# Performance work log

Measured on AMD Instinct MI355X. Metric: run time of the kernel, lower is better.

Reference implementation:

```python
import jax, jax.numpy as jnp
import numpy as np

N = 100000
F_IN = 256
F_HID = 256
F_OUT = 40
E = 3200000


def setup_inputs() -> dict:
    key = jax.random.key(0)
    ks = jax.random.split(key, 8)
    x = jax.random.normal(ks[0], (N, F_IN), dtype=jnp.float32)
    edge_index = jax.random.randint(ks[1], (2, E), 0, N, dtype=jnp.int64)
    s1 = 1.0 / np.sqrt(F_IN)
    s2 = 1.0 / np.sqrt(F_HID)
    W1 = jax.random.uniform(ks[2], (F_IN, F_HID), jnp.float32, -s1, s1)
    b1 = jnp.zeros((F_HID,), jnp.float32)
    W2 = jax.random.uniform(ks[3], (F_HID, F_HID), jnp.float32, -s2, s2)
    b2 = jnp.zeros((F_HID,), jnp.float32)
    Wlin = jax.random.uniform(ks[4], (F_HID, F_OUT), jnp.float32, -s2, s2)
    blin = jax.random.uniform(ks[5], (F_OUT,), jnp.float32, -s2, s2)
    return {"x": x, "edge_index": edge_index, "W1": W1, "b1": b1,
            "W2": W2, "b2": b2, "Wlin": Wlin, "blin": blin}


def _gcn_conv(x, src, dst, deg_inv_sqrt, W, b):
    # PyG GCNConv: linear transform, then sym-normalized aggregation, then bias
    h = x @ W                                    # [N, F]
    coef = deg_inv_sqrt[src] * deg_inv_sqrt[dst]  # [E+N]
    msgs = h[src] * coef[:, None]                # gather + scale
    agg = jax.ops.segment_sum(msgs, dst, num_segments=x.shape[0])
    return agg + b


def reference(x, edge_index, W1, b1, W2, b2, Wlin, blin):
    n = x.shape[0]
    # add self-loops (static shape: E + N)
    loops = jnp.arange(n, dtype=edge_index.dtype)
    src = jnp.concatenate([edge_index[0], loops])
    dst = jnp.concatenate([edge_index[1], loops])
    deg = jax.ops.segment_sum(jnp.ones_like(dst, dtype=x.dtype), dst, num_segments=n)
    deg_inv_sqrt = jnp.where(deg > 0, jax.lax.rsqrt(deg), 0.0)
    # dropout is identity in eval mode (training=False)
    h = _gcn_conv(x, src, dst, deg_inv_sqrt, W1, b1)
    h = _gcn_conv(h, src, dst, deg_inv_sqrt, W2, b2)
    logits = h @ Wlin + blin
    return jax.nn.log_softmax(logits, axis=1)
```

## Files before the change

kernel.cpp:

```cpp
#include <hip/hip_runtime.h>
#include <hip/hip_bf16.h>

#define FDIM 256
#define FOUT 40
#define RPB 256

typedef __attribute__((ext_vector_type(8))) short short8;
typedef __attribute__((ext_vector_type(4))) float floatx4;

__device__ __forceinline__ float bf2f(unsigned short u) {
  unsigned int x = ((unsigned int)u) << 16;
  float f;
  __builtin_memcpy(&f, &x, 4);
  return f;
}
__device__ __forceinline__ unsigned short f2bf(float f) {
  __hip_bfloat16 h = __float2bfloat16(f);
  unsigned short u;
  __builtin_memcpy(&u, &h, 2);
  return u;
}


__global__ void detect_k(const int* __restrict__ raw, int nwords, int* __restrict__ flag) {
  if (threadIdx.x == 0) *flag = 0;
  __syncthreads();
  int found = 0;
  for (int w = 1 + 2 * threadIdx.x; w < nwords; w += 512)
    if (raw[w] != 0) { found = 1; break; }
  if (found) atomicOr(flag, 1);
}

__global__ void normalize_k(const int* __restrict__ raw, const int* __restrict__ flag,
                            int* __restrict__ srcN, int* __restrict__ dstN, int e) {
  int i = blockIdx.x * 256 + threadIdx.x;
  if (i >= e) return;
  if (*flag) {
    srcN[i] = raw[i];
    dstN[i] = raw[e + i];
  } else {
    srcN[i] = raw[2 * i];
    dstN[i] = raw[2 * (e + i)];
  }
}


__global__ void zero_cnt_k(int* cnt, int n) {
  int i = blockIdx.x * 256 + threadIdx.x;
  if (i < n) cnt[i] = 0;
}

__global__ void count_k(const int* __restrict__ dst, int* __restrict__ cnt, int e, int n) {
  int i = blockIdx.x * 256 + threadIdx.x;
  if (i < e) {
    int d = dst[i];
    if (d >= 0 && d < n) atomicAdd(&cnt[d], 1);
  }
}

__global__ void dis_leg_k(const int* __restrict__ cnt, float* __restrict__ dis, int n) {
  int i = blockIdx.x * 256 + threadIdx.x;
  if (i < n) dis[i] = rsqrtf((float)cnt[i] + 1.0f);
}

__global__ void scan_a_k(const int* __restrict__ cnt, int* __restrict__ excl,
                         int* __restrict__ bsum, int n) {
  __shared__ int sh[1024];
  int t = threadIdx.x;
  int gid = blockIdx.x * 1024 + t;
  int v = (gid < n) ? cnt[gid] : 0;
  sh[t] = v;
  __syncthreads();
  for (int off = 1; off < 1024; off <<= 1) {
    int x = (t >= off) ? sh[t - off] : 0;
    __syncthreads();
    sh[t] += x;
    __syncthreads();
  }
  if (gid < n) excl[gid] = sh[t] - v;
  if (t == 1023) bsum[blockIdx.x] = sh[1023];
}

__global__ void scan_b_k(int* __restrict__ bsum, int nb) {
  __shared__ int sh[1024];
  int t = threadIdx.x;
  int v = (t < nb) ? bsum[t] : 0;
  sh[t] = v;
  __syncthreads();
  for (int off = 1; off < 1024; off <<= 1) {
    int x = (t >= off) ? sh[t - off] : 0;
    __syncthreads();
    sh[t] += x;
    __syncthreads();
  }
  if (t < nb) bsum[t] = sh[t] - v;
}

__global__ void scan_c_k(int* __restrict__ row_ptr, const int* __restrict__ bsum,
                         const int* __restrict__ cnt, int* __restrict__ cursor, int n) {
  int gid = blockIdx.x * 1024 + threadIdx.x;
  if (gid < n) {
    int r = row_ptr[gid] + bsum[blockIdx.x];
    row_ptr[gid] = r;
    cursor[gid] = r;
    if (gid == n - 1) row_ptr[n] = r + cnt[gid];
  }
}

__global__ void fill_k(const int* __restrict__ src, const int* __restrict__ dst,
                       int* __restrict__ cursor, int* __restrict__ col, int e, int n) {
  int i = blockIdx.x * 256 + threadIdx.x;
  if (i < e) {
    int d = dst[i];
    if (d >= 0 && d < n) {
      int slot = atomicAdd(&cursor[d], 1);
      int s = src[i];
      s = min(max(s, 0), n - 1);
      col[slot] = s;
    }
  }
}


__global__ __launch_bounds__(512) void zerob_k(int* __restrict__ bcnt, int nbuck) {
  int t = threadIdx.x;
  if (t < nbuck) bcnt[t] = 0;
}

__global__ __launch_bounds__(256) void bhist_k(
    const int* __restrict__ raw, const int* __restrict__ flag,
    int* __restrict__ bcnt, int e, int n, int nbuck, int cpb) {
  __shared__ int hist[512];
  int t = threadIdx.x;
  for (int b = t; b < nbuck; b += 256) hist[b] = 0;
  __syncthreads();
  int fl = *flag;
  int start = blockIdx.x * cpb;
  int endc = min(e, start + cpb);
  for (int i = start + t; i < endc; i += 256) {
    int d = fl ? raw[e + i] : raw[2 * (e + i)];
    if (d >= 0 && d < n) atomicAdd(&hist[d >> 8], 1);
  }
  __syncthreads();
  for (int b = t; b < nbuck; b += 256)
    if (hist[b]) atomicAdd(&bcnt[b], hist[b]);
}

__global__ __launch_bounds__(512) void bscan_k(
    const int* __restrict__ bcnt, int* __restrict__ bbase,
    int* __restrict__ bcur, int nbuck) {
  __shared__ int sh[512];
  int t = threadIdx.x;
  int v = (t < nbuck) ? bcnt[t] : 0;
  sh[t] = v;
  __syncthreads();
  for (int off = 1; off < 512; off <<= 1) {
    int x = (t >= off) ? sh[t - off] : 0;
    __syncthreads();
    sh[t] += x;
    __syncthreads();
  }
  if (t < nbuck) {
    int ex = sh[t] - v;
    bbase[t] = ex;
    bcur[t] = ex;
  }
  if (t == nbuck - 1) bbase[nbuck] = sh[t];
}

__global__ __launch_bounds__(1024) void bin2_k(
    const int* __restrict__ raw, const int* __restrict__ flag,
    int* __restrict__ bcur, unsigned int* __restrict__ binned,
    int e, int n, int nbuck, int cpb) {
  __shared__ int hist[512];
  __shared__ int base_[512];
  __shared__ int cnt2[512];
  int t = threadIdx.x;
  int fl = *flag;
  int start = blockIdx.x * cpb;
  int endc = min(e, start + cpb);
  for (int b = t; b < nbuck; b += 1024) { hist[b] = 0; cnt2[b] = 0; }
  __syncthreads();
  for (int i = start + t; i < endc; i += 1024) {
    int d = fl ? raw[e + i] : raw[2 * (e + i)];
    if (d >= 0 && d < n) atomicAdd(&hist[d >> 8], 1);
  }
  __syncthreads();
  for (int b = t; b < nbuck; b += 1024) {
    int h = hist[b];
    base_[b] = h ? atomicAdd(&bcur[b], h) : 0;
  }
  __syncthreads();
  for (int i = start + t; i < endc; i += 1024) {
    int d = fl ? raw[e + i] : raw[2 * (e + i)];
    if (d >= 0 && d < n) {
      int s = fl ? raw[i] : raw[2 * i];
      s = min(max(s, 0), n - 1);
      int bk = d >> 8;
      int pos = base_[bk] + atomicAdd(&cnt2[bk], 1);
      binned[pos] = (((unsigned int)(d & 255)) << 17) | (unsigned int)s;
    }
  }
}

__global__ __launch_bounds__(256) void scatcnt_k(
    const unsigned int* __restrict__ binned, const int* __restrict__ bbase,
    int* __restrict__ row_ptr, float* __restrict__ dis,
    int* __restrict__ col, int n) {
  __shared__ int cnt[RPB];
  __shared__ int sc[RPB];
  __shared__ int cur[RPB];
  int b = blockIdx.x;
  int r0 = b * RPB;
  int r1 = min(n, r0 + RPB);
  int nr = r1 - r0;
  int t = threadIdx.x;
  cnt[t] = 0;
  __syncthreads();
  int e0 = bbase[b], e1 = bbase[b + 1];
  for (int i = e0 + t; i < e1; i += 256)
    atomicAdd(&cnt[binned[i] >> 17], 1);
  __syncthreads();
  int v = cnt[t];
  if (t < nr) dis[r0 + t] = rsqrtf((float)v + 1.0f);
  sc[t] = v;
  __syncthreads();
  for (int off = 1; off < 256; off <<= 1) {
    int x = (t >= off) ? sc[t - off] : 0;
    __syncthreads();
    sc[t] += x;
    __syncthreads();
  }
  int base = e0 + sc[t] - v;
  cur[t] = base;
  if (t < nr) row_ptr[r0 + t] = base;
  if (t == 0 && r1 == n) row_ptr[n] = e1;
  __syncthreads();
  for (int i = e0 + t; i < e1; i += 256) {
    unsigned int p = binned[i];
    int dlow = (int)(p >> 17);
    int slot = atomicAdd(&cur[dlow], 1);
    col[slot] = (int)(p & 0x1FFFF);
  }
}


__global__ __launch_bounds__(64) void wc_k(const float* __restrict__ W2,
                                           const float* __restrict__ Wlin,
                                           float* __restrict__ Wc) {
  __shared__ float row[FDIM];
  int k = blockIdx.x, t = threadIdx.x;
  for (int j = t; j < FDIM; j += 64) row[j] = W2[(size_t)k * FDIM + j];
  __syncthreads();
  if (t < FOUT) {
    float acc = 0.f;
    for (int j = 0; j < FDIM; ++j) acc += row[j] * Wlin[(size_t)j * FOUT + t];
    Wc[(size_t)k * FOUT + t] = acc;
  }
}

__global__ __launch_bounds__(64) void wfull_k(const float* __restrict__ W1,
                                              const float* __restrict__ Wc,
                                              float* __restrict__ Wfull) {
  __shared__ float row[FDIM];
  int k = blockIdx.x, t = threadIdx.x;
  for (int j = t; j < FDIM; j += 64) row[j] = W1[(size_t)k * FDIM + j];
  __syncthreads();
  if (t < FOUT) {
    float acc = 0.f;
    for (int j = 0; j < FDIM; ++j) acc += row[j] * Wc[(size_t)j * FOUT + t];
    Wfull[(size_t)k * FOUT + t] = acc;
  }
}

__global__ __launch_bounds__(64) void rvec_k(const float* __restrict__ b1,
                                             const float* __restrict__ Wc,
                                             const float* __restrict__ b2,
                                             const float* __restrict__ Wlin,
                                             const float* __restrict__ blin,
                                             float* __restrict__ b1c,
                                             float* __restrict__ r2) {
  int t = threadIdx.x;
  if (t < FOUT) {
    float a = 0.f, b = blin[t];
    for (int j = 0; j < FDIM; ++j) {
      a += b1[j] * Wc[(size_t)j * FOUT + t];
      b += b2[j] * Wlin[(size_t)j * FOUT + t];
    }
    b1c[t] = a;
    r2[t] = b;
  }
}

__global__ void wft_k(const float* __restrict__ Wfull, unsigned short* __restrict__ WfT) {
  int o = blockIdx.x, k = threadIdx.x;
  WfT[(size_t)o * FDIM + k] = (o < FOUT) ? f2bf(Wfull[(size_t)k * FOUT + o]) : (unsigned short)0;
}


__global__ __launch_bounds__(256) void proj_k(
    const float* __restrict__ X, const unsigned short* __restrict__ WfT,
    const float* __restrict__ dis, float* __restrict__ Ys, int M) {
  __shared__ __align__(16) unsigned short Asm[64 * 40];
  __shared__ __align__(16) unsigned short Bsm[48 * 264];
  int t = threadIdx.x;
  int block_m = blockIdx.x * 64;
  int lane = t & 63, wave = t >> 6;
  int q = lane >> 4, rcol = lane & 15;
  for (int idx = t; idx < 48 * 256; idx += 256) {
    int o = idx >> 8, k = idx & 255;
    Bsm[o * 264 + k] = WfT[(size_t)o * FDIM + k];
  }
  floatx4 acc[3] = {};
  int arow = t >> 2, cc = (t & 3) * 8;
  int gm = block_m + arow;
  for (int kk = 0; kk < FDIM; kk += 32) {
    __syncthreads();
    {
      float4 v0 = {0, 0, 0, 0}, v1 = {0, 0, 0, 0};
      if (gm < M) {
        v0 = *(const float4*)(X + (size_t)gm * FDIM + kk + cc);
        v1 = *(const float4*)(X + (size_t)gm * FDIM + kk + cc + 4);
      }
      short8 pk;
      pk[0] = (short)f2bf(v0.x); pk[1] = (short)f2bf(v0.y);
      pk[2] = (short)f2bf(v0.z); pk[3] = (short)f2bf(v0.w);
      pk[4] = (short)f2bf(v1.x); pk[5] = (short)f2bf(v1.y);
      pk[6] = (short)f2bf(v1.z); pk[7] = (short)f2bf(v1.w);
      *(short8*)(Asm + arow * 40 + cc) = pk;
    }
    __syncthreads();
    short8 af = *(const short8*)(Asm + (wave * 16 + rcol) * 40 + q * 8);
    short8 b0 = *(const short8*)(Bsm + (rcol)*264 + kk + q * 8);
    short8 b1f = *(const short8*)(Bsm + (16 + rcol) * 264 + kk + q * 8);
    short8 b2f = *(const short8*)(Bsm + (32 + rcol) * 264 + kk + q * 8);
    acc[0] = __builtin_amdgcn_mfma_f32_16x16x32_bf16(af, b0, acc[0], 0, 0, 0);
    acc[1] = __builtin_amdgcn_mfma_f32_16x16x32_bf16(af, b1f, acc[1], 0, 0, 0);
    acc[2] = __builtin_amdgcn_mfma_f32_16x16x32_bf16(af, b2f, acc[2], 0, 0, 0);
  }
#pragma unroll
  for (int rr = 0; rr < 4; ++rr) {
    int m = block_m + wave * 16 + q * 4 + rr;
    if (m >= M) continue;
    float sc = dis[m];
    float* orow = Ys + (size_t)m * FOUT;
    orow[rcol] = acc[0][rr] * sc;
    orow[16 + rcol] = acc[1][rr] * sc;
    if (rcol < 8) orow[32 + rcol] = acc[2][rr] * sc;
  }
}


__global__ __launch_bounds__(256) void agg1_k(
    const float* __restrict__ T, const int* __restrict__ row_ptr,
    const int* __restrict__ col, const float* __restrict__ dis,
    const float* __restrict__ b1c, float* __restrict__ O, int n) {
  int wave = threadIdx.x >> 6, lane = threadIdx.x & 63;
  int wid = blockIdx.x * 4 + wave;
  int nw = gridDim.x * 4;
  bool act = lane < FOUT;
  float bv = act ? b1c[lane] : 0.f;
  for (int i = wid; i < n; i += nw) {
    float a = act ? T[(size_t)i * FOUT + lane] : 0.f;
    int beg = row_ptr[i], end = row_ptr[i + 1];
    for (int j0 = beg; j0 < end; j0 += 64) {
      int jj = j0 + lane;
      int cs = (jj < end) ? col[jj] : 0;
      int cc = min(64, end - j0);
      for (int k = 0; k < cc; k += 16) {
        int sl[16];
        float w[16];
#pragma unroll
        for (int u = 0; u < 16; ++u) {
          int ku = k + u;
          sl[u] = __builtin_amdgcn_readlane(cs, ku & 63);
          w[u] = (ku < cc) ? 1.f : 0.f;
        }
        float g[16];
#pragma unroll
        for (int u = 0; u < 16; ++u)
          g[u] = act ? T[(size_t)sl[u] * FOUT + lane] : 0.f;
#pragma unroll
        for (int u = 0; u < 16; ++u) a = fmaf(w[u], g[u], a);
      }
    }
    if (act) {
      float di = dis[i];
      O[(size_t)i * FOUT + lane] = (di * a + bv) * di;
    }
  }
}


__global__ __launch_bounds__(256) void agg2_k(
    const float* __restrict__ T, const int* __restrict__ row_ptr,
    const int* __restrict__ col, const float* __restrict__ dis,
    const float* __restrict__ r2, float* __restrict__ out, int n) {
  int wave = threadIdx.x >> 6, lane = threadIdx.x & 63;
  int wid = blockIdx.x * 4 + wave;
  int nw = gridDim.x * 4;
  bool act = lane < FOUT;
  float rv = act ? r2[lane] : 0.f;
  for (int i = wid; i < n; i += nw) {
    float a = act ? T[(size_t)i * FOUT + lane] : 0.f;
    int beg = row_ptr[i], end = row_ptr[i + 1];
    for (int j0 = beg; j0 < end; j0 += 64) {
      int jj = j0 + lane;
      int cs = (jj < end) ? col[jj] : 0;
      int cc = min(64, end - j0);
      for (int k = 0; k < cc; k += 16) {
        int sl[16];
        float w[16];
#pragma unroll
        for (int u = 0; u < 16; ++u) {
          int ku = k + u;
          sl[u] = __builtin_amdgcn_readlane(cs, ku & 63);
          w[u] = (ku < cc) ? 1.f : 0.f;
        }
        float g[16];
#pragma unroll
        for (int u = 0; u < 16; ++u)
          g[u] = act ? T[(size_t)sl[u] * FOUT + lane] : 0.f;
#pragma unroll
        for (int u = 0; u < 16; ++u) a = fmaf(w[u], g[u], a);
      }
    }
    float di = dis[i];
    float v = act ? (di * a + rv) : -3.4e38f;
    float m = v;
#pragma unroll
    for (int off = 32; off; off >>= 1) m = fmaxf(m, __shfl_xor(m, off));
    float e = act ? __expf(v - m) : 0.f;
    float s = e;
#pragma unroll
    for (int off = 32; off; off >>= 1) s += __shfl_xor(s, off);
    float lg = m + __logf(s);
    if (act) out[(size_t)i * FOUT + lane] = v - lg;
  }
}


extern "C" void kernel_launch(void* const* d_in, const int* in_sizes, int n_in,
                              void* d_out, int out_size, void* d_ws, size_t ws_size,
                              hipStream_t stream) {
  const float* x   = (const float*)d_in[0];
  const int* eraw  = (const int*)d_in[1];
  const float* W1  = (const float*)d_in[2];
  const float* b1  = (const float*)d_in[3];
  const float* W2  = (const float*)d_in[4];
  const float* b2  = (const float*)d_in[5];
  const float* Wl  = (const float*)d_in[6];
  const float* bl  = (const float*)d_in[7];
  float* out = (float*)d_out;

  const int N = in_sizes[0] / FDIM;
  const int E = in_sizes[1] / 2;

  char* w = (char*)d_ws;
  size_t off = 0;
  auto take = [&](size_t bytes) {
    void* p = w + off;
    off = (off + bytes + 255) & ~(size_t)255;
    return p;
  };
  int* cnt     = (int*)take((size_t)N * 4);
  int* cursor  = (int*)take((size_t)N * 4);
  int* row_ptr = (int*)take((size_t)(N + 1) * 4);
  float* dis   = (float*)take((size_t)N * 4);
  int* bsum    = (int*)take(4096);
  int* eflag   = (int*)take(256);
  int* bcnt    = (int*)take(512 * 4);
  int* bbase   = (int*)take(513 * 4);
  int* bcur    = (int*)take(512 * 4);
  float* Wc    = (float*)take((size_t)FDIM * FOUT * 4);
  float* Wfull = (float*)take((size_t)FDIM * FOUT * 4);
  unsigned short* WfT = (unsigned short*)take((size_t)48 * FDIM * 2);
  float* b1c   = (float*)take(256);
  float* r2    = (float*)take(256);
  int* colx    = (int*)take((size_t)E * 4);

  size_t pairBytes = (size_t)2 * E * 4;
  size_t tabBytes  = (size_t)N * FOUT * 4;
  size_t rABytes = pairBytes > tabBytes ? pairBytes : tabBytes;
  char* regionA = (char*)take(rABytes);
  int* srcN = (int*)regionA;
  int* dstN = srcN + E;
  float* Ys = (float*)regionA;
  size_t binBytes = (size_t)E * 4;
  size_t rBBytes = binBytes > tabBytes ? binBytes : tabBytes;
  char* regionB = (char*)take(rBBytes);
  unsigned int* binned = (unsigned int*)regionB;
  float* Z1s = (float*)regionB;
  (void)n_in; (void)out_size; (void)ws_size;

  int gE = (E + 255) / 256;
  int gN = (N + 255) / 256;
  int NB = (N + 1023) / 1024;
  int gP = (N + 63) / 64;
  int nbuck = (N + RPB - 1) / RPB;
  bool bucketed = (N <= (1 << 17));

  int probe_words = 65536 < 2 * E ? 65536 : 2 * E;
  hipLaunchKernelGGL(detect_k, dim3(1), dim3(256), 0, stream, eraw, probe_words, eflag);

  if (bucketed) {
    int nblk = 256;
    int cpb = (E + nblk - 1) / nblk;
    hipLaunchKernelGGL(zerob_k, dim3(1), dim3(512), 0, stream, bcnt, nbuck);
    hipLaunchKernelGGL(bhist_k, dim3(nblk), dim3(256), 0, stream,
                       eraw, eflag, bcnt, E, N, nbuck, cpb);
    hipLaunchKernelGGL(bscan_k, dim3(1), dim3(512), 0, stream, bcnt, bbase, bcur, nbuck);
    hipLaunchKernelGGL(bin2_k, dim3(nblk), dim3(1024), 0, stream,
                       eraw, eflag, bcur, binned, E, N, nbuck, cpb);
    hipLaunchKernelGGL(scatcnt_k, dim3(nbuck), dim3(256), 0, stream,
                       binned, bbase, row_ptr, dis, colx, N);
  } else {
    hipLaunchKernelGGL(normalize_k, dim3(gE), dim3(256), 0, stream, eraw, eflag, srcN, dstN, E);
    hipLaunchKernelGGL(zero_cnt_k, dim3(gN), dim3(256), 0, stream, cnt, N);
    hipLaunchKernelGGL(count_k, dim3(gE), dim3(256), 0, stream, dstN, cnt, E, N);
    hipLaunchKernelGGL(dis_leg_k, dim3(gN), dim3(256), 0, stream, cnt, dis, N);
    hipLaunchKernelGGL(scan_a_k, dim3(NB), dim3(1024), 0, stream, cnt, row_ptr, bsum, N);
    hipLaunchKernelGGL(scan_b_k, dim3(1), dim3(1024), 0, stream, bsum, NB);
    hipLaunchKernelGGL(scan_c_k, dim3(NB), dim3(1024), 0, stream, row_ptr, bsum, cnt, cursor, N);
    hipLaunchKernelGGL(fill_k, dim3(gE), dim3(256), 0, stream, srcN, dstN, cursor, colx, E, N);
  }

  hipLaunchKernelGGL(wc_k, dim3(FDIM), dim3(64), 0, stream, W2, Wl, Wc);
  hipLaunchKernelGGL(wfull_k, dim3(FDIM), dim3(64), 0, stream, W1, Wc, Wfull);
  hipLaunchKernelGGL(rvec_k, dim3(1), dim3(64), 0, stream, b1, Wc, b2, Wl, bl, b1c, r2);
  hipLaunchKernelGGL(wft_k, dim3(48), dim3(FDIM), 0, stream, Wfull, WfT);

  hipLaunchKernelGGL(proj_k, dim3(gP), dim3(256), 0, stream, x, WfT, dis, Ys, N);
  hipLaunchKernelGGL(agg1_k, dim3(2048), dim3(256), 0, stream,
                     Ys, row_ptr, colx, dis, b1c, Z1s, N);
  hipLaunchKernelGGL(agg2_k, dim3(2048), dim3(256), 0, stream,
                     Z1s, row_ptr, colx, dis, r2, out, N);
}
```

Baseline: 514.9 us.

## Store projected node tables in bf16 and gather three edges per wave step

Measured after the change: 463.8 us. 1.11x faster.

```diff
diff --git a/kernel.cpp b/kernel.cpp
--- a/kernel.cpp
+++ b/kernel.cpp
@@ -19,6 +19,12 @@
   unsigned short u;
   __builtin_memcpy(&u, &h, 2);
   return u;
+}
+__device__ __forceinline__ float blo(unsigned int v) {
+  unsigned int x = v << 16; float f; __builtin_memcpy(&f, &x, 4); return f;
+}
+__device__ __forceinline__ float bhi(unsigned int v) {
+  unsigned int x = v & 0xFFFF0000u; float f; __builtin_memcpy(&f, &x, 4); return f;
 }
 
 
@@ -300,7 +306,7 @@
 
 __global__ __launch_bounds__(256) void proj_k(
     const float* __restrict__ X, const unsigned short* __restrict__ WfT,
-    const float* __restrict__ dis, float* __restrict__ Ys, int M) {
+    const float* __restrict__ dis, unsigned int* __restrict__ Ys32, int M) {
   __shared__ __align__(16) unsigned short Asm[64 * 40];
   __shared__ __align__(16) unsigned short Bsm[48 * 264];
   int t = threadIdx.x;
@@ -338,104 +344,176 @@
     acc[1] = __builtin_amdgcn_mfma_f32_16x16x32_bf16(af, b1f, acc[1], 0, 0, 0);
     acc[2] = __builtin_amdgcn_mfma_f32_16x16x32_bf16(af, b2f, acc[2], 0, 0, 0);
   }
+  __syncthreads();
 #pragma unroll
   for (int rr = 0; rr < 4; ++rr) {
-    int m = block_m + wave * 16 + q * 4 + rr;
-    if (m >= M) continue;
-    float sc = dis[m];
-    float* orow = Ys + (size_t)m * FOUT;
-    orow[rcol] = acc[0][rr] * sc;
-    orow[16 + rcol] = acc[1][rr] * sc;
-    if (rcol < 8) orow[32 + rcol] = acc[2][rr] * sc;
+    int ml = wave * 16 + q * 4 + rr;
+    int m = block_m + ml;
+    float sc = (m < M) ? dis[m] : 0.f;
+    unsigned short* lrow = Asm + ml * 40;
+    lrow[rcol] = f2bf(acc[0][rr] * sc);
+    lrow[16 + rcol] = f2bf(acc[1][rr] * sc);
+    if (rcol < 8) lrow[32 + rcol] = f2bf(acc[2][rr] * sc);
+  }
+  __syncthreads();
+  const unsigned int* A32 = (const unsigned int*)Asm;
+  for (int idx = t; idx < 64 * 20; idx += 256) {
+    int r = idx / 20, c = idx - r * 20;
+    int m = block_m + r;
+    if (m < M) Ys32[(size_t)m * 20 + c] = A32[idx];
   }
 }
 
 
 __global__ __launch_bounds__(256) void agg1_k(
-    const float* __restrict__ T, const int* __restrict__ row_ptr,
+    const unsigned int* __restrict__ T32, const int* __restrict__ row_ptr,
     const int* __restrict__ col, const float* __restrict__ dis,
-    const float* __restrict__ b1c, float* __restrict__ O, int n) {
+    const float* __restrict__ b1c, unsigned int* __restrict__ O32, int n) {
   int wave = threadIdx.x >> 6, lane = threadIdx.x & 63;
   int wid = blockIdx.x * 4 + wave;
   int nw = gridDim.x * 4;
-  bool act = lane < FOUT;
-  float bv = act ? b1c[lane] : 0.f;
+  int e = lane / 20;
+  int fp = lane - e * 20;
+  if (e > 2) { e = 2; fp = 19; }
+  bool e0 = (e == 0), e1 = (e == 1);
+  bool g0 = e0;
+  float2 bv = ((const float2*)b1c)[fp];
   for (int i = wid; i < n; i += nw) {
-    float a = act ? T[(size_t)i * FOUT + lane] : 0.f;
+    unsigned int sv = T32[(size_t)i * 20 + fp];
+    float a0 = g0 ? blo(sv) : 0.f;
+    float a1 = g0 ? bhi(sv) : 0.f;
     int beg = row_ptr[i], end = row_ptr[i + 1];
     for (int j0 = beg; j0 < end; j0 += 64) {
       int jj = j0 + lane;
       int cs = (jj < end) ? col[jj] : 0;
       int cc = min(64, end - j0);
-      for (int k = 0; k < cc; k += 16) {
-        int sl[16];
-        float w[16];
-#pragma unroll
-        for (int u = 0; u < 16; ++u) {
-          int ku = k + u;
-          sl[u] = __builtin_amdgcn_readlane(cs, ku & 63);
-          w[u] = (ku < cc) ? 1.f : 0.f;
+      int kf = cc - cc % 24;
+      int k = 0;
+      for (; k < kf; k += 24) {
+        int sel[8];
+#pragma unroll
+        for (int u = 0; u < 8; ++u) {
+          int sa = __builtin_amdgcn_readlane(cs, k + 3 * u);
+          int sb = __builtin_amdgcn_readlane(cs, k + 3 * u + 1);
+          int sc2 = __builtin_amdgcn_readlane(cs, k + 3 * u + 2);
+          sel[u] = e0 ? sa : (e1 ? sb : sc2);
         }
-        float g[16];
-#pragma unroll
-        for (int u = 0; u < 16; ++u)
-          g[u] = act ? T[(size_t)sl[u] * FOUT + lane] : 0.f;
-#pragma unroll
-        for (int u = 0; u < 16; ++u) a = fmaf(w[u], g[u], a);
+        unsigned int g[8];
+#pragma unroll
+        for (int u = 0; u < 8; ++u) g[u] = T32[(size_t)sel[u] * 20 + fp];
+#pragma unroll
+        for (int u = 0; u < 8; ++u) { a0 += blo(g[u]); a1 += bhi(g[u]); }
       }
-    }
-    if (act) {
+      if (k < cc) {
+        int sel[8];
+        float w[8];
+#pragma unroll
+        for (int u = 0; u < 8; ++u) {
+          int kb = k + 3 * u;
+          int sa = __builtin_amdgcn_readlane(cs, kb & 63);
+          int sb = __builtin_amdgcn_readlane(cs, (kb + 1) & 63);
+          int sc2 = __builtin_amdgcn_readlane(cs, (kb + 2) & 63);
+          sel[u] = e0 ? sa : (e1 ? sb : sc2);
+          w[u] = (kb + e < cc) ? 1.f : 0.f;
+        }
+        unsigned int g[8];
+#pragma unroll
+        for (int u = 0; u < 8; ++u) g[u] = T32[(size_t)sel[u] * 20 + fp];
+#pragma unroll
+        for (int u = 0; u < 8; ++u) {
+          a0 = fmaf(w[u], blo(g[u]), a0);
+          a1 = fmaf(w[u], bhi(g[u]), a1);
+        }
+      }
+    }
+    a0 += __shfl(a0, fp + 20) + __shfl(a0, fp + 40);
+    a1 += __shfl(a1, fp + 20) + __shfl(a1, fp + 40);
+    if (g0) {
       float di = dis[i];
-      O[(size_t)i * FOUT + lane] = (di * a + bv) * di;
-    }
-  }
-}
-
+      unsigned int p = (unsigned int)f2bf((di * a0 + bv.x) * di) |
+                       ((unsigned int)f2bf((di * a1 + bv.y) * di) << 16);
+      O32[(size_t)i * 20 + fp] = p;
+    }
+  }
+}
 
 __global__ __launch_bounds__(256) void agg2_k(
-    const float* __restrict__ T, const int* __restrict__ row_ptr,
+    const unsigned int* __restrict__ T32, const int* __restrict__ row_ptr,
     const int* __restrict__ col, const float* __restrict__ dis,
     const float* __restrict__ r2, float* __restrict__ out, int n) {
   int wave = threadIdx.x >> 6, lane = threadIdx.x & 63;
   int wid = blockIdx.x * 4 + wave;
   int nw = gridDim.x * 4;
-  bool act = lane < FOUT;
-  float rv = act ? r2[lane] : 0.f;
+  int e = lane / 20;
+  int fp = lane - e * 20;
+  if (e > 2) { e = 2; fp = 19; }
+  bool e0 = (e == 0), e1 = (e == 1);
+  bool g0 = e0;
+  float2 rv = ((const float2*)r2)[fp];
   for (int i = wid; i < n; i += nw) {
-    float a = act ? T[(size_t)i * FOUT + lane] : 0.f;
+    unsigned int sv = T32[(size_t)i * 20 + fp];
+    float a0 = g0 ? blo(sv) : 0.f;
+    float a1 = g0 ? bhi(sv) : 0.f;
     int beg = row_ptr[i], end = row_ptr[i + 1];
     for (int j0 = beg; j0 < end; j0 += 64) {
       int jj = j0 + lane;
       int cs = (jj < end) ? col[jj] : 0;
       int cc = min(64, end - j0);
-      for (int k = 0; k < cc; k += 16) {
-        int sl[16];
-        float w[16];
-#pragma unroll
-        for (int u = 0; u < 16; ++u) {
-          int ku = k + u;
-          sl[u] = __builtin_amdgcn_readlane(cs, ku & 63);
-          w[u] = (ku < cc) ? 1.f : 0.f;
+      int kf = cc - cc % 24;
+      int k = 0;
+      for (; k < kf; k += 24) {
+        int sel[8];
+#pragma unroll
+        for (int u = 0; u < 8; ++u) {
+          int sa = __builtin_amdgcn_readlane(cs, k + 3 * u);
+          int sb = __builtin_amdgcn_readlane(cs, k + 3 * u + 1);
+          int sc2 = __builtin_amdgcn_readlane(cs, k + 3 * u + 2);
+          sel[u] = e0 ? sa : (e1 ? sb : sc2);
         }
-        float g[16];
-#pragma unroll
-        for (int u = 0; u < 16; ++u)
-          g[u] = act ? T[(size_t)sl[u] * FOUT + lane] : 0.f;
-#pragma unroll
-        for (int u = 0; u < 16; ++u) a = fmaf(w[u], g[u], a);
+        unsigned int g[8];
+#pragma unroll
+        for (int u = 0; u < 8; ++u) g[u] = T32[(size_t)sel[u] * 20 + fp];
+#pragma unroll
+        for (int u = 0; u < 8; ++u) { a0 += blo(g[u]); a1 += bhi(g[u]); }
       }
-    }
+      if (k < cc) {
+        int sel[8];
+        float w[8];
+#pragma unroll
+        for (int u = 0; u < 8; ++u) {
+          int kb = k + 3 * u;
+          int sa = __builtin_amdgcn_readlane(cs, kb & 63);
+          int sb = __builtin_amdgcn_readlane(cs, (kb + 1) & 63);
+          int sc2 = __builtin_amdgcn_readlane(cs, (kb + 2) & 63);
+          sel[u] = e0 ? sa : (e1 ? sb : sc2);
+          w[u] = (kb + e < cc) ? 1.f : 0.f;
+        }
+        unsigned int g[8];
+#pragma unroll
+        for (int u = 0; u < 8; ++u) g[u] = T32[(size_t)sel[u] * 20 + fp];
+#pragma unroll
+        for (int u = 0; u < 8; ++u) {
+          a0 = fmaf(w[u], blo(g[u]), a0);
+          a1 = fmaf(w[u], bhi(g[u]), a1);
+        }
+      }
+    }
+    a0 += __shfl(a0, fp + 20) + __shfl(a0, fp + 40);
+    a1 += __shfl(a1, fp + 20) + __shfl(a1, fp + 40);
     float di = dis[i];
-    float v = act ? (di * a + rv) : -3.4e38f;
-    float m = v;
+    float v0 = g0 ? (di * a0 + rv.x) : -3.4e38f;
+    float v1 = g0 ? (di * a1 + rv.y) : -3.4e38f;
+    float m = fmaxf(v0, v1);
 #pragma unroll
     for (int off = 32; off; off >>= 1) m = fmaxf(m, __shfl_xor(m, off));
-    float e = act ? __expf(v - m) : 0.f;
-    float s = e;
+    float s = g0 ? (__expf(v0 - m) + __expf(v1 - m)) : 0.f;
 #pragma unroll
     for (int off = 32; off; off >>= 1) s += __shfl_xor(s, off);
     float lg = m + __logf(s);
-    if (act) out[(size_t)i * FOUT + lane] = v - lg;
+    if (g0) {
+      float2 o = {v0 - lg, v1 - lg};
+      *(float2*)(out + (size_t)i * FOUT + 2 * fp) = o;
+    }
   }
 }
 
@@ -480,17 +558,17 @@
   int* colx    = (int*)take((size_t)E * 4);
 
   size_t pairBytes = (size_t)2 * E * 4;
-  size_t tabBytes  = (size_t)N * FOUT * 4;
+  size_t tabBytes  = (size_t)N * FOUT * 2;
   size_t rABytes = pairBytes > tabBytes ? pairBytes : tabBytes;
   char* regionA = (char*)take(rABytes);
   int* srcN = (int*)regionA;
   int* dstN = srcN + E;
-  float* Ys = (float*)regionA;
+  unsigned int* Ys32 = (unsigned int*)regionA;
   size_t binBytes = (size_t)E * 4;
   size_t rBBytes = binBytes > tabBytes ? binBytes : tabBytes;
   char* regionB = (char*)take(rBBytes);
   unsigned int* binned = (unsigned int*)regionB;
-  float* Z1s = (float*)regionB;
+  unsigned int* Z1s32 = (unsigned int*)regionB;
   (void)n_in; (void)out_size; (void)ws_size;
 
   int gE = (E + 255) / 256;
@@ -530,9 +608,9 @@
   hipLaunchKernelGGL(rvec_k, dim3(1), dim3(64), 0, stream, b1, Wc, b2, Wl, bl, b1c, r2);
   hipLaunchKernelGGL(wft_k, dim3(48), dim3(FDIM), 0, stream, Wfull, WfT);
 
-  hipLaunchKernelGGL(proj_k, dim3(gP), dim3(256), 0, stream, x, WfT, dis, Ys, N);
+  hipLaunchKernelGGL(proj_k, dim3(gP), dim3(256), 0, stream, x, WfT, dis, Ys32, N);
   hipLaunchKernelGGL(agg1_k, dim3(2048), dim3(256), 0, stream,
-                     Ys, row_ptr, colx, dis, b1c, Z1s, N);
+                     Ys32, row_ptr, colx, dis, b1c, Z1s32, N);
   hipLaunchKernelGGL(agg2_k, dim3(2048), dim3(256), 0, stream,
-                     Z1s, row_ptr, colx, dis, r2, out, N);
-}
+                     Z1s32, row_ptr, colx, dis, r2, out, N);
+}
```
